# Kernel tuning notes

Measured on AMD Instinct MI355X. Metric: run time of the kernel, lower is better.

Reference implementation:

```python
import jax, jax.numpy as jnp
import numpy as np

N, D = 8192, 256

def _gram_rbf(x, y, sigma):
    x2 = jnp.sum(x * x, axis=-1)                      # [N]
    y2 = jnp.sum(y * y, axis=-1)                      # [M]
    xy = jnp.einsum('nd,md->nm', x, y)                # [N,M] GEMM
    sq = x2[:, None] + y2[None, :] - 2.0 * xy
    return jnp.exp(-sq / sigma)

def setup_inputs() -> dict:
    key = jax.random.key(0)
    k1, k2 = jax.random.split(key)
    return {
        'input': jax.random.normal(k1, (N, D), dtype=jnp.float32),
        'target': jax.random.normal(k2, (N, D), dtype=jnp.float32) + 0.5,
        'sigma': 256,
    }

def reference(input, target, sigma):
    XX = _gram_rbf(input, input, sigma)
    YY = _gram_rbf(target, target, sigma)
    XY = _gram_rbf(input, target, sigma)
    return jnp.mean(XX) + jnp.mean(YY) - 2.0 * jnp.mean(XY)
```

## Files before the change

kernel.cpp:

```cpp
#include <hip/hip_runtime.h>
#include <hip/hip_bf16.h>
#include <stdint.h>
#include <stddef.h>


#define N_PTS   8192
#define DIM     256
#define TWO_N   16384
#define CSTRIDE 16

#define AS1 __attribute__((address_space(1)))
#define AS3 __attribute__((address_space(3)))

typedef __attribute__((ext_vector_type(4))) float f32x4;
typedef __attribute__((ext_vector_type(4))) int   i32x4;
typedef __attribute__((ext_vector_type(8))) int   i32x8;

__global__ __launch_bounds__(256) void mmd_prep(const float* __restrict__ X,
                                                const float* __restrict__ Y,
                                                const int* __restrict__ sigmap,
                                                unsigned char* __restrict__ Zf8,
                                                float* __restrict__ n2,
                                                float* __restrict__ out) {
    if (blockIdx.x == 0 && threadIdx.x == 0) out[0] = 0.0f;

    const int wave = threadIdx.x >> 6;
    const int lane = threadIdx.x & 63;
    const int row  = blockIdx.x * 4 + wave;

    const float* src = (row < N_PTS) ? (X + (size_t)row * DIM)
                                     : (Y + (size_t)(row - N_PTS) * DIM);
    float4 v = ((const float4*)src)[lane];

    float s = v.x * v.x + v.y * v.y + v.z * v.z + v.w * v.w;
#pragma unroll
    for (int off = 32; off; off >>= 1) s += __shfl_down(s, off, 64);
    if (lane == 0) {
        const float c2 = -1.4426950408889634f / (float)(*sigmap);
        n2[row] = c2 * s;
    }

    const int p01 = __builtin_amdgcn_cvt_pk_fp8_f32(v.x, v.y, 0, false);
    const int p23 = __builtin_amdgcn_cvt_pk_fp8_f32(v.z, v.w, 0, false);
    const unsigned int pk = ((unsigned)p01 & 0xffffu) | ((unsigned)p23 << 16);
    *(unsigned int*)(Zf8 + (size_t)row * DIM + (size_t)lane * 4) = pk;
}

__global__ __launch_bounds__(256, 4) void mmd_main(const unsigned char* __restrict__ Zf8,
                                                   const float* __restrict__ n2,
                                                   const int* __restrict__ sigmap,
                                                   float* __restrict__ out) {
    __shared__ char smem_b[32768];
    __shared__ float wsum[4];

    const int bid = (int)blockIdx.x;
    const int br  = 127 - (bid >> 4);
    const int cc  = bid & 15;
    if (cc > br) return;

    const int t    = threadIdx.x;
    const int wave = t >> 6;
    const int lane = t & 63;
    const int g    = lane >> 4;
    const int ml   = lane & 15;
    const int rowBase = br * 128;

    const float m2 = 2.8853900817779268f / (float)(*sigmap);
    const int   SC = 0x7f7f7f7f;

    const int gbase = (t >> 4) * 256 + (((t & 15) ^ (t >> 4)) * 16);
    const int lbase = t * 16;

    int rb0[2], rb1[2];
#pragma unroll
    for (int kc = 0; kc < 2; ++kc) {
        rb0[kc] = ml * 256 + (((kc * 8 + g * 2)     ^ ml) * 16);
        rb1[kc] = ml * 256 + (((kc * 8 + g * 2 + 1) ^ ml) * 16);
    }

    i32x8 af[2][2];
#pragma unroll
    for (int mt = 0; mt < 2; ++mt) {
        const unsigned char* rp =
            Zf8 + (size_t)(rowBase + wave * 32 + mt * 16 + ml) * 256 + g * 32;
#pragma unroll
        for (int kc = 0; kc < 2; ++kc) {
            union { i32x4 h[2]; i32x8 v; } u;
            u.h[0] = *(const i32x4*)(rp + kc * 128);
            u.h[1] = *(const i32x4*)(rp + kc * 128 + 16);
            af[mt][kc] = u.v;
        }
    }
    float a_i[2][4];
#pragma unroll
    for (int mt = 0; mt < 2; ++mt)
#pragma unroll
        for (int rr = 0; rr < 4; ++rr)
            a_i[mt][rr] = n2[rowBase + wave * 32 + mt * 16 + g * 4 + rr];

    const f32x4 zacc = {0.0f, 0.0f, 0.0f, 0.0f};

    {
        const unsigned char* sb = Zf8 + (size_t)cc * 128 * 256 + gbase;
#pragma unroll
        for (int i = 0; i < 4; ++i)
            __builtin_amdgcn_global_load_lds((const AS1 void*)(sb + i * 4096),
                                             (AS3 void*)(smem_b + i * 4096 + lbase), 16, 0, 0);
    }

    float block_acc = 0.0f;
    const int brX = (br < 64);
    const int nT  = (br - cc) / CSTRIDE + 1;
    const int nS  = nT * 2;
    int cur = 0;

    for (int ss = 0; ss < nS; ++ss) {
        const int bc = cc + (ss >> 1) * CSTRIDE;
        const int h  = ss & 1;
        const int colBase = bc * 128 + h * 64;

        float eb[4];
#pragma unroll
        for (int nt = 0; nt < 4; ++nt)
            eb[nt] = __builtin_amdgcn_exp2f(n2[colBase + nt * 16 + ml]);

        __syncthreads();

        if (ss + 1 < nS) {
            const int bcN = cc + ((ss + 1) >> 1) * CSTRIDE;
            const int hN  = (ss + 1) & 1;
            const unsigned char* sb =
                Zf8 + (size_t)(bcN * 128 + hN * 64) * 256 + gbase;
            char* dst = smem_b + (cur ^ 1) * 16384;
#pragma unroll
            for (int i = 0; i < 4; ++i)
                __builtin_amdgcn_global_load_lds((const AS1 void*)(sb + i * 4096),
                                                 (AS3 void*)(dst + i * 4096 + lbase), 16, 0, 0);
        }

        const char* buf = smem_b + cur * 16384;
        f32x4 acc[2][4];
#pragma unroll
        for (int nt = 0; nt < 4; ++nt) {
#pragma unroll
            for (int kc = 0; kc < 2; ++kc) {
                union { i32x4 h[2]; i32x8 v; } u;
                u.h[0] = *(const i32x4*)(buf + nt * 4096 + rb0[kc]);
                u.h[1] = *(const i32x4*)(buf + nt * 4096 + rb1[kc]);
                const i32x8 bf = u.v;
#pragma unroll
                for (int mt = 0; mt < 2; ++mt)
                    acc[mt][nt] = __builtin_amdgcn_mfma_scale_f32_16x16x128_f8f6f4(
                        af[mt][kc], bf, (kc == 0) ? zacc : acc[mt][nt],
                        0, 0, 0, SC, 0, SC);
            }
        }

        float ts0 = 0.0f, ts1 = 0.0f, ts2 = 0.0f, ts3 = 0.0f;
#pragma unroll
        for (int mt = 0; mt < 2; ++mt)
#pragma unroll
            for (int nt = 0; nt < 4; ++nt) {
                const float e = eb[nt];
                ts0 = fmaf(__builtin_amdgcn_exp2f(fmaf(acc[mt][nt][0], m2, a_i[mt][0])), e, ts0);
                ts1 = fmaf(__builtin_amdgcn_exp2f(fmaf(acc[mt][nt][1], m2, a_i[mt][1])), e, ts1);
                ts2 = fmaf(__builtin_amdgcn_exp2f(fmaf(acc[mt][nt][2], m2, a_i[mt][2])), e, ts2);
                ts3 = fmaf(__builtin_amdgcn_exp2f(fmaf(acc[mt][nt][3], m2, a_i[mt][3])), e, ts3);
            }
        const float tsum = (ts0 + ts1) + (ts2 + ts3);

        const float sgn = ((bc < 64) == brX) ? 1.0f : -1.0f;
        const float w   = (bc == br) ? sgn : 2.0f * sgn;
        block_acc = fmaf(w, tsum, block_acc);
        cur ^= 1;
    }

    float s = block_acc;
#pragma unroll
    for (int off = 32; off; off >>= 1) s += __shfl_down(s, off, 64);
    if (lane == 0) wsum[wave] = s;
    __syncthreads();
    if (t == 0)
        atomicAdd(out, (wsum[0] + wsum[1] + wsum[2] + wsum[3]) * (1.0f / 67108864.0f));
}

extern "C" void kernel_launch(void* const* d_in, const int* in_sizes, int n_in,
                              void* d_out, int out_size, void* d_ws, size_t ws_size,
                              hipStream_t stream) {
    const float* X      = (const float*)d_in[0];
    const float* Y      = (const float*)d_in[1];
    const int*   sigmap = (const int*)d_in[2];
    float*       out    = (float*)d_out;

    unsigned char* Zf8 = (unsigned char*)d_ws;
    float*         n2  = (float*)((char*)d_ws + (size_t)TWO_N * DIM);

    mmd_prep<<<TWO_N / 4, 256, 0, stream>>>(X, Y, sigmap, Zf8, n2, out);
    mmd_main<<<128 * CSTRIDE, 256, 0, stream>>>(Zf8, n2, sigmap, out);
}
```

Measured before the change: 113.8 us.

## Launch one block per lower-triangular tile and reduce via partial atomic slots

```diff
diff --git a/kernel.cpp b/kernel.cpp
--- a/kernel.cpp
+++ b/kernel.cpp
@@ -7,7 +7,7 @@
 #define N_PTS   8192
 #define DIM     256
 #define TWO_N   16384
-#define CSTRIDE 16
+#define NTILE   8256
 
 #define AS1 __attribute__((address_space(1)))
 #define AS3 __attribute__((address_space(3)))
@@ -21,8 +21,8 @@
                                                 const int* __restrict__ sigmap,
                                                 unsigned char* __restrict__ Zf8,
                                                 float* __restrict__ n2,
-                                                float* __restrict__ out) {
-    if (blockIdx.x == 0 && threadIdx.x == 0) out[0] = 0.0f;
+                                                float* __restrict__ part) {
+    if (blockIdx.x == 0 && threadIdx.x < 64) part[threadIdx.x] = 0.0f;
 
     const int wave = threadIdx.x >> 6;
     const int lane = threadIdx.x & 63;
@@ -49,14 +49,17 @@
 __global__ __launch_bounds__(256, 4) void mmd_main(const unsigned char* __restrict__ Zf8,
                                                    const float* __restrict__ n2,
                                                    const int* __restrict__ sigmap,
-                                                   float* __restrict__ out) {
+                                                   float* __restrict__ part) {
     __shared__ char smem_b[32768];
     __shared__ float wsum[4];
 
-    const int bid = (int)blockIdx.x;
-    const int br  = 127 - (bid >> 4);
-    const int cc  = bid & 15;
-    if (cc > br) return;
+    const int r = (int)blockIdx.x;
+    int k = (int)((__builtin_sqrt(8.0 * (double)r + 1.0) - 1.0) * 0.5);
+    int base = (k * (k + 1)) >> 1;
+    if (r < base)                { --k; base = (k * (k + 1)) >> 1; }
+    else if (r >= base + k + 1)  { ++k; base = (k * (k + 1)) >> 1; }
+    const int br = k;
+    const int cc = r - base;
 
     const int t    = threadIdx.x;
     const int wave = t >> 6;
@@ -68,14 +71,14 @@
     const float m2 = 2.8853900817779268f / (float)(*sigmap);
     const int   SC = 0x7f7f7f7f;
 
-    const int gbase = (t >> 4) * 256 + (((t & 15) ^ (t >> 4)) * 16);
-    const int lbase = t * 16;
-
-    int rb0[2], rb1[2];
+    {
+        const int gbase = (t >> 4) * 256 + (((t & 15) ^ ((t >> 4) & 15)) * 16);
+        const unsigned char* sb = Zf8 + (size_t)cc * 32768 + gbase;
+        const int lbase = t * 16;
 #pragma unroll
-    for (int kc = 0; kc < 2; ++kc) {
-        rb0[kc] = ml * 256 + (((kc * 8 + g * 2)     ^ ml) * 16);
-        rb1[kc] = ml * 256 + (((kc * 8 + g * 2 + 1) ^ ml) * 16);
+        for (int i = 0; i < 8; ++i)
+            __builtin_amdgcn_global_load_lds((const AS1 void*)(sb + i * 4096),
+                                             (AS3 void*)(smem_b + i * 4096 + lbase), 16, 0, 0);
     }
 
     i32x8 af[2][2];
@@ -98,55 +101,33 @@
         for (int rr = 0; rr < 4; ++rr)
             a_i[mt][rr] = n2[rowBase + wave * 32 + mt * 16 + g * 4 + rr];
 
+    float eb[8];
+#pragma unroll
+    for (int j = 0; j < 8; ++j)
+        eb[j] = __builtin_amdgcn_exp2f(n2[cc * 128 + j * 16 + ml]);
+
+    int rb0[2], rb1[2];
+#pragma unroll
+    for (int kc = 0; kc < 2; ++kc) {
+        rb0[kc] = ml * 256 + (((kc * 8 + g * 2)     ^ ml) * 16);
+        rb1[kc] = ml * 256 + (((kc * 8 + g * 2 + 1) ^ ml) * 16);
+    }
+
     const f32x4 zacc = {0.0f, 0.0f, 0.0f, 0.0f};
 
-    {
-        const unsigned char* sb = Zf8 + (size_t)cc * 128 * 256 + gbase;
+    __syncthreads();
+
+    float ts0 = 0.0f, ts1 = 0.0f, ts2 = 0.0f, ts3 = 0.0f;
 #pragma unroll
-        for (int i = 0; i < 4; ++i)
-            __builtin_amdgcn_global_load_lds((const AS1 void*)(sb + i * 4096),
-                                             (AS3 void*)(smem_b + i * 4096 + lbase), 16, 0, 0);
-    }
-
-    float block_acc = 0.0f;
-    const int brX = (br < 64);
-    const int nT  = (br - cc) / CSTRIDE + 1;
-    const int nS  = nT * 2;
-    int cur = 0;
-
-    for (int ss = 0; ss < nS; ++ss) {
-        const int bc = cc + (ss >> 1) * CSTRIDE;
-        const int h  = ss & 1;
-        const int colBase = bc * 128 + h * 64;
-
-        float eb[4];
-#pragma unroll
-        for (int nt = 0; nt < 4; ++nt)
-            eb[nt] = __builtin_amdgcn_exp2f(n2[colBase + nt * 16 + ml]);
-
-        __syncthreads();
-
-        if (ss + 1 < nS) {
-            const int bcN = cc + ((ss + 1) >> 1) * CSTRIDE;
-            const int hN  = (ss + 1) & 1;
-            const unsigned char* sb =
-                Zf8 + (size_t)(bcN * 128 + hN * 64) * 256 + gbase;
-            char* dst = smem_b + (cur ^ 1) * 16384;
-#pragma unroll
-            for (int i = 0; i < 4; ++i)
-                __builtin_amdgcn_global_load_lds((const AS1 void*)(sb + i * 4096),
-                                                 (AS3 void*)(dst + i * 4096 + lbase), 16, 0, 0);
-        }
-
-        const char* buf = smem_b + cur * 16384;
+    for (int h = 0; h < 2; ++h) {
         f32x4 acc[2][4];
 #pragma unroll
         for (int nt = 0; nt < 4; ++nt) {
 #pragma unroll
             for (int kc = 0; kc < 2; ++kc) {
-                union { i32x4 h[2]; i32x8 v; } u;
-                u.h[0] = *(const i32x4*)(buf + nt * 4096 + rb0[kc]);
-                u.h[1] = *(const i32x4*)(buf + nt * 4096 + rb1[kc]);
+                union { i32x4 hh[2]; i32x8 v; } u;
+                u.hh[0] = *(const i32x4*)(smem_b + h * 16384 + nt * 4096 + rb0[kc]);
+                u.hh[1] = *(const i32x4*)(smem_b + h * 16384 + nt * 4096 + rb1[kc]);
                 const i32x8 bf = u.v;
 #pragma unroll
                 for (int mt = 0; mt < 2; ++mt)
@@ -155,33 +136,37 @@
                         0, 0, 0, SC, 0, SC);
             }
         }
-
-        float ts0 = 0.0f, ts1 = 0.0f, ts2 = 0.0f, ts3 = 0.0f;
 #pragma unroll
         for (int mt = 0; mt < 2; ++mt)
 #pragma unroll
             for (int nt = 0; nt < 4; ++nt) {
-                const float e = eb[nt];
+                const float e = eb[h * 4 + nt];
                 ts0 = fmaf(__builtin_amdgcn_exp2f(fmaf(acc[mt][nt][0], m2, a_i[mt][0])), e, ts0);
                 ts1 = fmaf(__builtin_amdgcn_exp2f(fmaf(acc[mt][nt][1], m2, a_i[mt][1])), e, ts1);
                 ts2 = fmaf(__builtin_amdgcn_exp2f(fmaf(acc[mt][nt][2], m2, a_i[mt][2])), e, ts2);
                 ts3 = fmaf(__builtin_amdgcn_exp2f(fmaf(acc[mt][nt][3], m2, a_i[mt][3])), e, ts3);
             }
-        const float tsum = (ts0 + ts1) + (ts2 + ts3);
-
-        const float sgn = ((bc < 64) == brX) ? 1.0f : -1.0f;
-        const float w   = (bc == br) ? sgn : 2.0f * sgn;
-        block_acc = fmaf(w, tsum, block_acc);
-        cur ^= 1;
     }
 
-    float s = block_acc;
+    const float sgn = ((cc < 64) == (br < 64)) ? 1.0f : -1.0f;
+    const float w   = (cc == br) ? sgn : 2.0f * sgn;
+    float s = w * ((ts0 + ts1) + (ts2 + ts3));
+
 #pragma unroll
     for (int off = 32; off; off >>= 1) s += __shfl_down(s, off, 64);
     if (lane == 0) wsum[wave] = s;
     __syncthreads();
     if (t == 0)
-        atomicAdd(out, (wsum[0] + wsum[1] + wsum[2] + wsum[3]) * (1.0f / 67108864.0f));
+        atomicAdd(part + (r & 63), wsum[0] + wsum[1] + wsum[2] + wsum[3]);
+}
+
+__global__ __launch_bounds__(64) void mmd_finish(const float* __restrict__ part,
+                                                 float* __restrict__ out) {
+    const int lane = threadIdx.x & 63;
+    float s = part[lane];
+#pragma unroll
+    for (int off = 32; off; off >>= 1) s += __shfl_down(s, off, 64);
+    if (lane == 0) out[0] = s * (1.0f / 67108864.0f);
 }
 
 extern "C" void kernel_launch(void* const* d_in, const int* in_sizes, int n_in,
@@ -192,9 +177,11 @@
     const int*   sigmap = (const int*)d_in[2];
     float*       out    = (float*)d_out;
 
-    unsigned char* Zf8 = (unsigned char*)d_ws;
-    float*         n2  = (float*)((char*)d_ws + (size_t)TWO_N * DIM);
+    unsigned char* Zf8  = (unsigned char*)d_ws;
+    float*         n2   = (float*)((char*)d_ws + (size_t)TWO_N * DIM);
+    float*         part = n2 + TWO_N;
 
-    mmd_prep<<<TWO_N / 4, 256, 0, stream>>>(X, Y, sigmap, Zf8, n2, out);
-    mmd_main<<<128 * CSTRIDE, 256, 0, stream>>>(Zf8, n2, sigmap, out);
+    mmd_prep<<<TWO_N / 4, 256, 0, stream>>>(X, Y, sigmap, Zf8, n2, part);
+    mmd_main<<<NTILE, 256, 0, stream>>>(Zf8, n2, sigmap, part);
+    mmd_finish<<<1, 64, 0, stream>>>(part, out);
 }
```

Measured after the change: 124.4 us. 9.3% more time.

## Pair row tiles per block for balanced triangle work and spread atomics

Applied to the files above, without the earlier changes.

```diff
diff --git a/kernel.cpp b/kernel.cpp
--- a/kernel.cpp
+++ b/kernel.cpp
@@ -7,7 +7,6 @@
 #define N_PTS   8192
 #define DIM     256
 #define TWO_N   16384
-#define CSTRIDE 16
 
 #define AS1 __attribute__((address_space(1)))
 #define AS3 __attribute__((address_space(3)))
@@ -21,8 +20,8 @@
                                                 const int* __restrict__ sigmap,
                                                 unsigned char* __restrict__ Zf8,
                                                 float* __restrict__ n2,
-                                                float* __restrict__ out) {
-    if (blockIdx.x == 0 && threadIdx.x == 0) out[0] = 0.0f;
+                                                float* __restrict__ part) {
+    if (blockIdx.x == 0 && threadIdx.x < 64) part[threadIdx.x] = 0.0f;
 
     const int wave = threadIdx.x >> 6;
     const int lane = threadIdx.x & 63;
@@ -49,21 +48,26 @@
 __global__ __launch_bounds__(256, 4) void mmd_main(const unsigned char* __restrict__ Zf8,
                                                    const float* __restrict__ n2,
                                                    const int* __restrict__ sigmap,
-                                                   float* __restrict__ out) {
+                                                   float* __restrict__ part) {
     __shared__ char smem_b[32768];
     __shared__ float wsum[4];
 
     const int bid = (int)blockIdx.x;
-    const int br  = 127 - (bid >> 4);
+    const int p   = bid >> 4;
     const int cc  = bid & 15;
-    if (cc > br) return;
+    const int r0  = p;
+    const int r1  = 127 - p;
+
+    const int nT0 = (cc <= r0) ? (((r0 - cc) >> 4) + 1) : 0;
+    const int nT1 = ((r1 - cc) >> 4) + 1;
+    const int nS0 = nT0 * 2;
+    const int nS  = nS0 + nT1 * 2;
 
     const int t    = threadIdx.x;
     const int wave = t >> 6;
     const int lane = t & 63;
     const int g    = lane >> 4;
     const int ml   = lane & 15;
-    const int rowBase = br * 128;
 
     const float m2 = 2.8853900817779268f / (float)(*sigmap);
     const int   SC = 0x7f7f7f7f;
@@ -79,29 +83,46 @@
     }
 
     i32x8 af[2][2];
-#pragma unroll
-    for (int mt = 0; mt < 2; ++mt) {
-        const unsigned char* rp =
-            Zf8 + (size_t)(rowBase + wave * 32 + mt * 16 + ml) * 256 + g * 32;
-#pragma unroll
-        for (int kc = 0; kc < 2; ++kc) {
-            union { i32x4 h[2]; i32x8 v; } u;
-            u.h[0] = *(const i32x4*)(rp + kc * 128);
-            u.h[1] = *(const i32x4*)(rp + kc * 128 + 16);
-            af[mt][kc] = u.v;
+    float a_i[2][4];
+    auto loadA = [&](int rowTile) {
+        const int rowBase = rowTile * 128;
+#pragma unroll
+        for (int mt = 0; mt < 2; ++mt) {
+            const unsigned char* rp =
+                Zf8 + (size_t)(rowBase + wave * 32 + mt * 16 + ml) * 256 + g * 32;
+#pragma unroll
+            for (int kc = 0; kc < 2; ++kc) {
+                union { i32x4 h[2]; i32x8 v; } u;
+                u.h[0] = *(const i32x4*)(rp + kc * 128);
+                u.h[1] = *(const i32x4*)(rp + kc * 128 + 16);
+                af[mt][kc] = u.v;
+            }
         }
-    }
-    float a_i[2][4];
-#pragma unroll
-    for (int mt = 0; mt < 2; ++mt)
-#pragma unroll
-        for (int rr = 0; rr < 4; ++rr)
-            a_i[mt][rr] = n2[rowBase + wave * 32 + mt * 16 + g * 4 + rr];
+#pragma unroll
+        for (int mt = 0; mt < 2; ++mt)
+#pragma unroll
+            for (int rr = 0; rr < 4; ++rr)
+                a_i[mt][rr] = n2[rowBase + wave * 32 + mt * 16 + g * 4 + rr];
+    };
+
+    const int firstRow = nT0 ? r0 : r1;
+    loadA(firstRow);
+    int curRow = firstRow;
 
     const f32x4 zacc = {0.0f, 0.0f, 0.0f, 0.0f};
 
+    auto sliceCol = [&](int s, int& rowT, int& bc, int& h) {
+        int si;
+        if (s < nS0) { rowT = r0; si = s; }
+        else         { rowT = r1; si = s - nS0; }
+        bc = cc + (si >> 2) * 16 * 2;
+        bc = cc + ((si >> 1) * 16);
+        h  = si & 1;
+    };
+
     {
-        const unsigned char* sb = Zf8 + (size_t)cc * 128 * 256 + gbase;
+        int rT, bc, h; sliceCol(0, rT, bc, h);
+        const unsigned char* sb = Zf8 + (size_t)(bc * 128 + h * 64) * 256 + gbase;
 #pragma unroll
         for (int i = 0; i < 4; ++i)
             __builtin_amdgcn_global_load_lds((const AS1 void*)(sb + i * 4096),
@@ -109,14 +130,12 @@
     }
 
     float block_acc = 0.0f;
-    const int brX = (br < 64);
-    const int nT  = (br - cc) / CSTRIDE + 1;
-    const int nS  = nT * 2;
     int cur = 0;
 
-    for (int ss = 0; ss < nS; ++ss) {
-        const int bc = cc + (ss >> 1) * CSTRIDE;
-        const int h  = ss & 1;
+    for (int s = 0; s < nS; ++s) {
+        int rowT, bc, h;
+        sliceCol(s, rowT, bc, h);
+        if (rowT != curRow) { loadA(rowT); curRow = rowT; }
         const int colBase = bc * 128 + h * 64;
 
         float eb[4];
@@ -126,9 +145,9 @@
 
         __syncthreads();
 
-        if (ss + 1 < nS) {
-            const int bcN = cc + ((ss + 1) >> 1) * CSTRIDE;
-            const int hN  = (ss + 1) & 1;
+        if (s + 1 < nS) {
+            int rTN, bcN, hN;
+            sliceCol(s + 1, rTN, bcN, hN);
             const unsigned char* sb =
                 Zf8 + (size_t)(bcN * 128 + hN * 64) * 256 + gbase;
             char* dst = smem_b + (cur ^ 1) * 16384;
@@ -144,9 +163,9 @@
         for (int nt = 0; nt < 4; ++nt) {
 #pragma unroll
             for (int kc = 0; kc < 2; ++kc) {
-                union { i32x4 h[2]; i32x8 v; } u;
-                u.h[0] = *(const i32x4*)(buf + nt * 4096 + rb0[kc]);
-                u.h[1] = *(const i32x4*)(buf + nt * 4096 + rb1[kc]);
+                union { i32x4 hh[2]; i32x8 v; } u;
+                u.hh[0] = *(const i32x4*)(buf + nt * 4096 + rb0[kc]);
+                u.hh[1] = *(const i32x4*)(buf + nt * 4096 + rb1[kc]);
                 const i32x8 bf = u.v;
 #pragma unroll
                 for (int mt = 0; mt < 2; ++mt)
@@ -169,8 +188,8 @@
             }
         const float tsum = (ts0 + ts1) + (ts2 + ts3);
 
-        const float sgn = ((bc < 64) == brX) ? 1.0f : -1.0f;
-        const float w   = (bc == br) ? sgn : 2.0f * sgn;
+        const float sgn = ((bc < 64) == (rowT < 64)) ? 1.0f : -1.0f;
+        const float w   = (bc == rowT) ? sgn : 2.0f * sgn;
         block_acc = fmaf(w, tsum, block_acc);
         cur ^= 1;
     }
@@ -181,7 +200,16 @@
     if (lane == 0) wsum[wave] = s;
     __syncthreads();
     if (t == 0)
-        atomicAdd(out, (wsum[0] + wsum[1] + wsum[2] + wsum[3]) * (1.0f / 67108864.0f));
+        atomicAdd(part + (bid & 63), wsum[0] + wsum[1] + wsum[2] + wsum[3]);
+}
+
+__global__ __launch_bounds__(64) void mmd_finish(const float* __restrict__ part,
+                                                 float* __restrict__ out) {
+    const int lane = threadIdx.x & 63;
+    float s = part[lane];
+#pragma unroll
+    for (int off = 32; off; off >>= 1) s += __shfl_down(s, off, 64);
+    if (lane == 0) out[0] = s * (1.0f / 67108864.0f);
 }
 
 extern "C" void kernel_launch(void* const* d_in, const int* in_sizes, int n_in,
@@ -192,9 +220,11 @@
     const int*   sigmap = (const int*)d_in[2];
     float*       out    = (float*)d_out;
 
-    unsigned char* Zf8 = (unsigned char*)d_ws;
-    float*         n2  = (float*)((char*)d_ws + (size_t)TWO_N * DIM);
-
-    mmd_prep<<<TWO_N / 4, 256, 0, stream>>>(X, Y, sigmap, Zf8, n2, out);
-    mmd_main<<<128 * CSTRIDE, 256, 0, stream>>>(Zf8, n2, sigmap, out);
-}
+    unsigned char* Zf8  = (unsigned char*)d_ws;
+    float*         n2   = (float*)((char*)d_ws + (size_t)TWO_N * DIM);
+    float*         part = n2 + TWO_N;
+
+    mmd_prep<<<TWO_N / 4, 256, 0, stream>>>(X, Y, sigmap, Zf8, n2, part);
+    mmd_main<<<64 * 16, 256, 0, stream>>>(Zf8, n2, sigmap, part);
+    mmd_finish<<<1, 64, 0, stream>>>(part, out);
+}
```

Result: no change. 114.1 us (+0.3%).
